# Optimization experiments

Measured on AMD Instinct MI355X. Metric: run time of the kernel, lower is better.

Reference implementation:

```python
import jax, jax.numpy as jnp
import numpy as np

B, S = 64, 256           # batch, seq_len
V, E = 50000, 256        # vocab, embedding dim
H, L = 256, 9            # lstm hidden, num labels


def setup_inputs() -> dict:
    key = jax.random.key(0)
    ks = jax.random.split(key, 12)
    inputs = jax.random.randint(ks[0], (B, S), 0, V, dtype=jnp.int32)
    attention_mask = jnp.ones((B, S), dtype=jnp.int32)
    label = jax.random.randint(ks[1], (B, S), 0, L, dtype=jnp.int32)
    emb = jax.random.normal(ks[2], (V, E), jnp.float32) * 0.02
    # LSTM weights, keras gate order: i, f, g(cell), o stacked along last axis
    W_fwd = jax.random.normal(ks[3], (E, 4 * H), jnp.float32) * 0.05
    U_fwd = jax.random.normal(ks[4], (H, 4 * H), jnp.float32) * 0.05
    b_fwd = jnp.zeros((4 * H,), jnp.float32)
    W_bwd = jax.random.normal(ks[5], (E, 4 * H), jnp.float32) * 0.05
    U_bwd = jax.random.normal(ks[6], (H, 4 * H), jnp.float32) * 0.05
    b_bwd = jnp.zeros((4 * H,), jnp.float32)
    W_dense = jax.random.normal(ks[7], (2 * H, L), jnp.float32) * 0.05
    b_dense = jnp.zeros((L,), jnp.float32)
    trans = jax.random.uniform(ks[8], (L, L), jnp.float32)  # tf.random.uniform init
    return dict(inputs=inputs, attention_mask=attention_mask, label=label,
                emb=emb, W_fwd=W_fwd, U_fwd=U_fwd, b_fwd=b_fwd,
                W_bwd=W_bwd, U_bwd=U_bwd, b_bwd=b_bwd,
                W_dense=W_dense, b_dense=b_dense, trans=trans)


def _lstm(x, W, U, b):
    # x: [B,S,E] -> h sequence [B,S,H]; keras default activations (sigmoid/tanh)
    Bx = x.shape[0]
    Hd = U.shape[0]
    xz = jnp.einsum('bse,ef->bsf', x, W) + b  # precompute input projection

    def step(carry, zt):
        h, c = carry
        z = zt + h @ U
        i, f, g, o = jnp.split(z, 4, axis=-1)
        c = jax.nn.sigmoid(f) * c + jax.nn.sigmoid(i) * jnp.tanh(g)
        h = jax.nn.sigmoid(o) * jnp.tanh(c)
        return (h, c), h

    init = (jnp.zeros((Bx, Hd), x.dtype), jnp.zeros((Bx, Hd), x.dtype))
    _, hs = jax.lax.scan(step, init, jnp.swapaxes(xz, 0, 1))
    return jnp.swapaxes(hs, 0, 1)


def _crf_log_likelihood(logits, tags, lengths, trans):
    # logits [B,S,L], tags [B,S] int, lengths [B] int, trans [L,L]
    Bx, Sx, Lx = logits.shape
    t_idx = jnp.arange(Sx)
    valid = (t_idx[None, :] < lengths[:, None]).astype(logits.dtype)  # [B,S]
    unary = jnp.take_along_axis(logits, tags[..., None], axis=-1)[..., 0]
    unary_score = jnp.sum(unary * valid, axis=1)
    pair_valid = (t_idx[None, :Sx - 1] < (lengths[:, None] - 1)).astype(logits.dtype)
    binary = trans[tags[:, :-1], tags[:, 1:]]
    binary_score = jnp.sum(binary * pair_valid, axis=1)

    # forward algorithm (log-space), masked so alpha is carried through padding
    alpha0 = logits[:, 0]  # [B,L]

    def step(alpha, inp):
        emit, m = inp  # emit [B,L], m [B] bool
        new = jax.nn.logsumexp(alpha[:, :, None] + trans[None], axis=1) + emit
        alpha = jnp.where(m[:, None], new, alpha)
        return alpha, None

    emits = jnp.swapaxes(logits[:, 1:], 0, 1)               # [S-1,B,L]
    masks = jnp.swapaxes(t_idx[None, 1:] < lengths[:, None], 0, 1)
    alpha, _ = jax.lax.scan(step, alpha0, (emits, masks))
    log_norm = jax.nn.logsumexp(alpha, axis=-1)
    return unary_score + binary_score - log_norm


def reference(inputs, attention_mask, label, emb, W_fwd, U_fwd, b_fwd,
              W_bwd, U_bwd, b_bwd, W_dense, b_dense, trans):
    x = emb[inputs]  # [B,S,E]; dropout is identity at inference (training=None)
    h_f = _lstm(x, W_fwd, U_fwd, b_fwd)
    h_b = _lstm(x[:, ::-1], W_bwd, U_bwd, b_bwd)[:, ::-1]
    h = jnp.concatenate([h_f, h_b], axis=-1)  # [B,S,2H]
    logits = h @ W_dense + b_dense            # [B,S,L]
    lengths = jnp.sum((attention_mask != 0).astype(jnp.int32), axis=1)
    log_likelihood = _crf_log_likelihood(logits, label, lengths, trans)
    return logits, log_likelihood, trans
```

## Files before the change

kernel.cpp:

```cpp
#include <hip/hip_runtime.h>
#include <hip/hip_fp16.h>

typedef _Float16 half2_t __attribute__((ext_vector_type(2)));
typedef unsigned int u32;

constexpr int Bn = 64, Sn = 256, Ln = 9;
constexpr int G4H = 1024;

constexpr size_t XZ_OFF   = 0;
constexpr size_t XZ_BYTES = (size_t)2 * Bn * Sn * G4H * 4;
constexpr size_t H_OFF    = XZ_OFF + XZ_BYTES;
constexpr size_t H_BYTES  = (size_t)Bn * Sn * 512 * 4;
constexpr size_t UPK_OFF  = H_OFF + H_BYTES;
constexpr size_t UPK_BYTES= (size_t)2 * 128 * G4H * 4;

constexpr int PV = 96;
constexpr int PL = 32;

__device__ __forceinline__ float sigf(float x) {
  return __fdividef(1.0f, 1.0f + __expf(-x));
}
__device__ __forceinline__ float tanhf_fast(float x) {
  x = fminf(fmaxf(x, -15.0f), 15.0f);
  float e = __expf(-2.0f * x);
  return __fdividef(1.0f - e, 1.0f + e);
}

#if __has_builtin(__builtin_amdgcn_fdot2)
__device__ __forceinline__ float FDOT2(half2_t a, half2_t b, float c) {
  return __builtin_amdgcn_fdot2(a, b, c, false);
}
#else
__device__ __forceinline__ float FDOT2(half2_t a, half2_t b, float c) {
  return c + (float)a.x * (float)b.x + (float)a.y * (float)b.y;
}
#endif

__device__ __forceinline__ half2_t H2(u32 w) { return __builtin_bit_cast(half2_t, w); }

__global__ void pack_u(const float* __restrict__ Uf, const float* __restrict__ Ub,
                       u32* __restrict__ upk) {
  int idx = blockIdx.x * 256 + threadIdx.x;
  if (idx >= 2 * 128 * 1024) return;
  int d  = idx >> 17;
  int kp = (idx >> 10) & 127;
  int j  = idx & 1023;
  const float* U = d ? Ub : Uf;
  _Float16 a = (_Float16)U[(size_t)(2 * kp) * 1024 + j];
  _Float16 b = (_Float16)U[(size_t)(2 * kp + 1) * 1024 + j];
  u32 pa = (u32)__builtin_bit_cast(unsigned short, a);
  u32 pb = (u32)__builtin_bit_cast(unsigned short, b);
  upk[idx] = pa | (pb << 16);
}

__global__ __launch_bounds__(256, 4)
void xz_gemm(const int* __restrict__ tok, const float* __restrict__ emb,
             const float* __restrict__ Wf, const float* __restrict__ biasf,
             const float* __restrict__ Wb, const float* __restrict__ biasb,
             float* __restrict__ xz) {
  __shared__ float As[32][64];
  __shared__ float Bs[32][128];
  __shared__ int toks[64];
  const int tid = threadIdx.x;
  const int mt = blockIdx.x, nt = blockIdx.y;
  const int d = nt >> 3;
  const float* W    = d ? Wb : Wf;
  const float* bias = d ? biasb : biasf;
  const int n0 = (nt & 7) * 128;
  const int r0 = mt * 64;
  if (tid < 64) toks[tid] = tok[r0 + tid];
  __syncthreads();
  const int tr = tid >> 4, tc = tid & 15;
  float acc[4][8];
#pragma unroll
  for (int j = 0; j < 8; ++j) {
    float bv = bias[n0 + tc * 8 + j];
#pragma unroll
    for (int i = 0; i < 4; ++i) acc[i][j] = bv;
  }
  const int ai = tid >> 2, kq = tid & 3;
  const int kb = tid >> 3, fb = tid & 7;
  for (int k0 = 0; k0 < 256; k0 += 32) {
    const float* ar = emb + (size_t)toks[ai] * 256 + k0 + kq * 8;
    float4 a0 = *(const float4*)ar;
    float4 a1 = *(const float4*)(ar + 4);
    As[kq * 8 + 0][ai] = a0.x; As[kq * 8 + 1][ai] = a0.y;
    As[kq * 8 + 2][ai] = a0.z; As[kq * 8 + 3][ai] = a0.w;
    As[kq * 8 + 4][ai] = a1.x; As[kq * 8 + 5][ai] = a1.y;
    As[kq * 8 + 6][ai] = a1.z; As[kq * 8 + 7][ai] = a1.w;
    const float* wr = W + (size_t)(k0 + kb) * 1024 + n0;
#pragma unroll
    for (int q = 0; q < 4; ++q)
      *(float4*)&Bs[kb][(fb + 8 * q) * 4] = *(const float4*)(wr + (fb + 8 * q) * 4);
    __syncthreads();
#pragma unroll
    for (int kk = 0; kk < 32; ++kk) {
      float4 a4 = *(const float4*)&As[kk][tr * 4];
      float4 b0 = *(const float4*)&Bs[kk][tc * 8];
      float4 b1 = *(const float4*)&Bs[kk][tc * 8 + 4];
      float av[4] = {a4.x, a4.y, a4.z, a4.w};
      float bv[8] = {b0.x, b0.y, b0.z, b0.w, b1.x, b1.y, b1.z, b1.w};
#pragma unroll
      for (int i = 0; i < 4; ++i)
#pragma unroll
        for (int j = 0; j < 8; ++j) acc[i][j] += av[i] * bv[j];
    }
    __syncthreads();
  }
#pragma unroll
  for (int i = 0; i < 4; ++i) {
    int r = r0 + tr * 4 + i;
    int bb_ = r >> 8, s = r & 255;
    float* dst = xz + ((size_t)(d * 64 + bb_) * 256 + s) * 1024 + n0 + tc * 8;
    float4 o0 = {acc[i][0], acc[i][1], acc[i][2], acc[i][3]};
    float4 o1 = {acc[i][4], acc[i][5], acc[i][6], acc[i][7]};
    *(float4*)dst = o0;
    *(float4*)(dst + 4) = o1;
  }
}

__global__ __launch_bounds__(512)
void lstm_seq(const float* __restrict__ xz, const u32* __restrict__ upk,
              float* __restrict__ h_out) {
  const int seq = blockIdx.x;
  const int dir = seq >> 6;
  const int tid = threadIdx.x;
  const int colA = tid;
  const int colB = tid + 512;

  __shared__ uint4 ul[2 * (PL / 4) * 512];
  __shared__ float zbuf[1024];
  __shared__ __align__(16) u32 h2[128];

  const u32* ubase = upk + (size_t)dir * 131072;

  half2_t uA[PV], uB[PV];
#pragma unroll
  for (int kp = 0; kp < PV; ++kp) {
    uA[kp] = H2(ubase[(size_t)kp * 1024 + colA]);
    uB[kp] = H2(ubase[(size_t)kp * 1024 + colB]);
  }
#pragma unroll
  for (int q = 0; q < PL / 4; ++q) {
    uint4 va, vb;
    va.x = ubase[(size_t)(PV + 4 * q + 0) * 1024 + colA];
    va.y = ubase[(size_t)(PV + 4 * q + 1) * 1024 + colA];
    va.z = ubase[(size_t)(PV + 4 * q + 2) * 1024 + colA];
    va.w = ubase[(size_t)(PV + 4 * q + 3) * 1024 + colA];
    vb.x = ubase[(size_t)(PV + 4 * q + 0) * 1024 + colB];
    vb.y = ubase[(size_t)(PV + 4 * q + 1) * 1024 + colB];
    vb.z = ubase[(size_t)(PV + 4 * q + 2) * 1024 + colB];
    vb.w = ubase[(size_t)(PV + 4 * q + 3) * 1024 + colB];
    ul[q * 512 + tid] = va;
    ul[(PL / 4 + q) * 512 + tid] = vb;
  }
  if (tid < 128) h2[tid] = 0u;
  float c = 0.0f;

  const float* xzp = xz + (size_t)seq * 256 * 1024;
  float* hop = h_out + (size_t)(seq & 63) * 256 * 512 + dir * 256 + tid;
  __syncthreads();

  float xA = xzp[(size_t)(dir ? 255 : 0) * 1024 + colA];
  float xB = xzp[(size_t)(dir ? 255 : 0) * 1024 + colB];

  for (int t = 0; t < 256; ++t) {
    const int snext = (t < 255) ? (dir ? (254 - t) : (t + 1)) : (dir ? 255 : 0);
    float nA = xzp[(size_t)snext * 1024 + colA];
    float nB = xzp[(size_t)snext * 1024 + colB];

    float accA = xA, accB = xB;
#pragma unroll
    for (int q = 0; q < PV / 4; ++q) {
      uint4 hh = *(const uint4*)&h2[4 * q];
      accA = FDOT2(H2(hh.x), uA[4 * q + 0], accA);
      accA = FDOT2(H2(hh.y), uA[4 * q + 1], accA);
      accA = FDOT2(H2(hh.z), uA[4 * q + 2], accA);
      accA = FDOT2(H2(hh.w), uA[4 * q + 3], accA);
      accB = FDOT2(H2(hh.x), uB[4 * q + 0], accB);
      accB = FDOT2(H2(hh.y), uB[4 * q + 1], accB);
      accB = FDOT2(H2(hh.z), uB[4 * q + 2], accB);
      accB = FDOT2(H2(hh.w), uB[4 * q + 3], accB);
    }
#pragma unroll
    for (int q = 0; q < PL / 4; ++q) {
      uint4 hh = *(const uint4*)&h2[PV + 4 * q];
      uint4 va = ul[q * 512 + tid];
      uint4 vb = ul[(PL / 4 + q) * 512 + tid];
      accA = FDOT2(H2(hh.x), H2(va.x), accA);
      accA = FDOT2(H2(hh.y), H2(va.y), accA);
      accA = FDOT2(H2(hh.z), H2(va.z), accA);
      accA = FDOT2(H2(hh.w), H2(va.w), accA);
      accB = FDOT2(H2(hh.x), H2(vb.x), accB);
      accB = FDOT2(H2(hh.y), H2(vb.y), accB);
      accB = FDOT2(H2(hh.z), H2(vb.z), accB);
      accB = FDOT2(H2(hh.w), H2(vb.w), accB);
    }
    zbuf[colA] = accA;
    zbuf[colB] = accB;
    __syncthreads();

    const int s = dir ? (255 - t) : t;
    if (tid < 256) {
      float zi = zbuf[tid], zf = zbuf[tid + 256], zg = zbuf[tid + 512], zo = zbuf[tid + 768];
      c = sigf(zf) * c + sigf(zi) * tanhf_fast(zg);
      float h = sigf(zo) * tanhf_fast(c);
      hop[(size_t)s * 512] = h;
      ((_Float16*)h2)[tid] = (_Float16)h;
    }
    __syncthreads();
    xA = nA; xB = nB;
  }
}

__global__ __launch_bounds__(256, 4)
void logits_k(const float* __restrict__ h_out, const float* __restrict__ Wd,
              const float* __restrict__ bd, float* __restrict__ out) {
  __shared__ float Ws[512 * 9];
  __shared__ float bs[16];
  const int tid = threadIdx.x;
  for (int i = tid; i < 4608; i += 256) Ws[i] = Wd[i];
  if (tid < 9) bs[tid] = bd[tid];
  __syncthreads();
  const int w = tid >> 6, lane = tid & 63;
  const int r0 = blockIdx.x * 16 + w * 4;
  for (int rr = 0; rr < 4; ++rr) {
    const int r = r0 + rr;
    const float* hp = h_out + (size_t)r * 512 + lane * 8;
    float4 h0 = *(const float4*)hp;
    float4 h1 = *(const float4*)(hp + 4);
    float hv[8] = {h0.x, h0.y, h0.z, h0.w, h1.x, h1.y, h1.z, h1.w};
    float outv = 0.0f;
#pragma unroll
    for (int l = 0; l < 9; ++l) {
      float p = 0.0f;
#pragma unroll
      for (int uu = 0; uu < 8; ++uu) p += hv[uu] * Ws[(lane * 8 + uu) * 9 + l];
      for (int off = 32; off; off >>= 1) p += __shfl_xor(p, off, 64);
      if (lane == l) outv = p;
    }
    if (lane < 9) out[(size_t)r * 9 + lane] = outv + bs[lane];
  }
}

__global__ void crf_k(const float* __restrict__ logits, const int* __restrict__ label,
                      const int* __restrict__ mask, const float* __restrict__ trans,
                      float* __restrict__ out_ll, float* __restrict__ out_trans) {
  const int b = blockIdx.x;
  const int lane = threadIdx.x;
  int cnt = 0;
#pragma unroll
  for (int q = 0; q < 4; ++q) cnt += (mask[b * 256 + lane + q * 64] != 0) ? 1 : 0;
  for (int off = 32; off; off >>= 1) cnt += __shfl_xor(cnt, off, 64);
  const int len = cnt;
  float un = 0.0f;
#pragma unroll
  for (int q = 0; q < 4; ++q) {
    int s = lane + q * 64;
    if (s < len) un += logits[((size_t)b * 256 + s) * 9 + label[b * 256 + s]];
  }
  for (int off = 32; off; off >>= 1) un += __shfl_xor(un, off, 64);
  float bin = 0.0f;
#pragma unroll
  for (int q = 0; q < 4; ++q) {
    int s = lane + q * 64;
    if (s < 255 && s < len - 1)
      bin += trans[label[b * 256 + s] * 9 + label[b * 256 + s + 1]];
  }
  for (int off = 32; off; off >>= 1) bin += __shfl_xor(bin, off, 64);
  float alpha = (lane < 9) ? logits[((size_t)b * 256) * 9 + lane] : -INFINITY;
  float tcol[9];
  if (lane < 9) {
#pragma unroll
    for (int i = 0; i < 9; ++i) tcol[i] = trans[i * 9 + lane];
  }
  for (int t = 1; t < 256; ++t) {
    float a[9];
#pragma unroll
    for (int i = 0; i < 9; ++i) a[i] = __shfl(alpha, i, 64);
    if (lane < 9) {
      float mx = a[0] + tcol[0];
#pragma unroll
      for (int i = 1; i < 9; ++i) mx = fmaxf(mx, a[i] + tcol[i]);
      float ssum = 0.0f;
#pragma unroll
      for (int i = 0; i < 9; ++i) ssum += __expf(a[i] + tcol[i] - mx);
      float nw = mx + __logf(ssum) + logits[((size_t)b * 256 + t) * 9 + lane];
      if (t < len) alpha = nw;
    }
  }
  float mx = alpha;
  for (int off = 32; off; off >>= 1) mx = fmaxf(mx, __shfl_xor(mx, off, 64));
  float e = __expf(alpha - mx);
  for (int off = 32; off; off >>= 1) e += __shfl_xor(e, off, 64);
  if (lane == 0) out_ll[b] = un + bin - (mx + __logf(e));
  if (b == 0) {
    for (int i = lane; i < 81; i += 64) out_trans[i] = trans[i];
  }
}

extern "C" void kernel_launch(void* const* d_in, const int* in_sizes, int n_in,
                              void* d_out, int out_size, void* d_ws, size_t ws_size,
                              hipStream_t stream) {
  (void)in_sizes; (void)n_in; (void)out_size; (void)ws_size;
  const int*   inputs = (const int*)d_in[0];
  const int*   amask  = (const int*)d_in[1];
  const int*   label  = (const int*)d_in[2];
  const float* emb    = (const float*)d_in[3];
  const float* Wf     = (const float*)d_in[4];
  const float* Uf     = (const float*)d_in[5];
  const float* bf     = (const float*)d_in[6];
  const float* Wb     = (const float*)d_in[7];
  const float* Ub     = (const float*)d_in[8];
  const float* bb     = (const float*)d_in[9];
  const float* Wd     = (const float*)d_in[10];
  const float* bd     = (const float*)d_in[11];
  const float* trans  = (const float*)d_in[12];

  char* ws = (char*)d_ws;
  float* xz    = (float*)(ws + XZ_OFF);
  float* h_out = (float*)(ws + H_OFF);
  u32*   upk   = (u32*)(ws + UPK_OFF);

  float* out      = (float*)d_out;
  float* out_ll   = out + (size_t)Bn * Sn * Ln;
  float* out_tr   = out_ll + Bn;

  pack_u<<<1024, 256, 0, stream>>>(Uf, Ub, upk);
  xz_gemm<<<dim3(256, 16), 256, 0, stream>>>(inputs, emb, Wf, bf, Wb, bb, xz);
  lstm_seq<<<128, 512, 0, stream>>>(xz, upk, h_out);
  logits_k<<<1024, 256, 0, stream>>>(h_out, Wd, bd, out);
  crf_k<<<64, 64, 0, stream>>>(out, label, amask, trans, out_ll, out_tr);
}
```

Baseline: 783.1 us.

## Split LSTM recurrent matvec across 4-lane K groups with swizzled h buffer

Each thread now owns 8 gate columns over a quarter of the hidden dimension instead of 2 full columns. Six of those columns' weights stay in registers and two sit in LDS, and the partial sums are combined with cross-lane shuffles. The fp16 hidden-state buffer is stored in a swizzled layout so each lane group reads distinct 16-byte chunks, avoiding LDS bank conflicts on the broadcast reads. The xz input is loaded as float4 vectors. The aim is more register reuse of each loaded h chunk and fewer LDS reads per step, at the cost of shuffle-reduction overhead and a fixed waves-per-EU hint.

```diff
diff --git a/kernel.cpp b/kernel.cpp
--- a/kernel.cpp
+++ b/kernel.cpp
@@ -14,9 +14,6 @@
 constexpr size_t UPK_OFF  = H_OFF + H_BYTES;
 constexpr size_t UPK_BYTES= (size_t)2 * 128 * G4H * 4;
 
-constexpr int PV = 96;
-constexpr int PL = 32;
-
 __device__ __forceinline__ float sigf(float x) {
   return __fdividef(1.0f, 1.0f + __expf(-x));
 }
@@ -37,6 +34,10 @@
 #endif
 
 __device__ __forceinline__ half2_t H2(u32 w) { return __builtin_bit_cast(half2_t, w); }
+
+__device__ __forceinline__ int swz_g(int g) {
+  return (g & 24) | ((g + 2 * (g >> 3)) & 7);
+}
 
 __global__ void pack_u(const float* __restrict__ Uf, const float* __restrict__ Ub,
                        u32* __restrict__ upk) {
@@ -120,96 +121,115 @@
 }
 
 __global__ __launch_bounds__(512)
+__attribute__((amdgpu_waves_per_eu(2, 2)))
 void lstm_seq(const float* __restrict__ xz, const u32* __restrict__ upk,
               float* __restrict__ h_out) {
   const int seq = blockIdx.x;
   const int dir = seq >> 6;
   const int tid = threadIdx.x;
-  const int colA = tid;
-  const int colB = tid + 512;
-
-  __shared__ uint4 ul[2 * (PL / 4) * 512];
+  const int w    = tid >> 6;
+  const int lane = tid & 63;
+  const int kb   = lane & 3;
+  const int cb   = lane >> 2;
+  const int c0   = w * 128 + cb * 8;
+
+  __shared__ uint4 ul[16][512];
   __shared__ float zbuf[1024];
   __shared__ __align__(16) u32 h2[128];
 
-  const u32* ubase = upk + (size_t)dir * 131072;
-
-  half2_t uA[PV], uB[PV];
-#pragma unroll
-  for (int kp = 0; kp < PV; ++kp) {
-    uA[kp] = H2(ubase[(size_t)kp * 1024 + colA]);
-    uB[kp] = H2(ubase[(size_t)kp * 1024 + colB]);
-  }
-#pragma unroll
-  for (int q = 0; q < PL / 4; ++q) {
-    uint4 va, vb;
-    va.x = ubase[(size_t)(PV + 4 * q + 0) * 1024 + colA];
-    va.y = ubase[(size_t)(PV + 4 * q + 1) * 1024 + colA];
-    va.z = ubase[(size_t)(PV + 4 * q + 2) * 1024 + colA];
-    va.w = ubase[(size_t)(PV + 4 * q + 3) * 1024 + colA];
-    vb.x = ubase[(size_t)(PV + 4 * q + 0) * 1024 + colB];
-    vb.y = ubase[(size_t)(PV + 4 * q + 1) * 1024 + colB];
-    vb.z = ubase[(size_t)(PV + 4 * q + 2) * 1024 + colB];
-    vb.w = ubase[(size_t)(PV + 4 * q + 3) * 1024 + colB];
-    ul[q * 512 + tid] = va;
-    ul[(PL / 4 + q) * 512 + tid] = vb;
-  }
+  const u32* ub = upk + (size_t)dir * 131072;
+
+  half2_t uu[6][32];
+#pragma unroll
+  for (int j = 0; j < 6; ++j)
+#pragma unroll
+    for (int q = 0; q < 32; ++q)
+      uu[j][q] = H2(ub[(size_t)(32 * kb + q) * 1024 + (c0 + j)]);
+#pragma unroll
+  for (int j = 0; j < 6; ++j)
+#pragma unroll
+    for (int q = 0; q < 32; ++q)
+      asm volatile("" : "+v"(uu[j][q]));
+
+#pragma unroll
+  for (int cl = 0; cl < 2; ++cl)
+#pragma unroll
+    for (int s = 0; s < 8; ++s) {
+      uint4 v;
+      v.x = ub[(size_t)(32 * kb + 4 * s + 0) * 1024 + (c0 + 6 + cl)];
+      v.y = ub[(size_t)(32 * kb + 4 * s + 1) * 1024 + (c0 + 6 + cl)];
+      v.z = ub[(size_t)(32 * kb + 4 * s + 2) * 1024 + (c0 + 6 + cl)];
+      v.w = ub[(size_t)(32 * kb + 4 * s + 3) * 1024 + (c0 + 6 + cl)];
+      ul[cl * 8 + s][tid] = v;
+    }
   if (tid < 128) h2[tid] = 0u;
+
+  const char* h2b = (const char*)h2;
+  int hhoff[8];
+#pragma unroll
+  for (int s = 0; s < 8; ++s)
+    hhoff[s] = 16 * ((kb << 3) | ((s + 2 * kb) & 7));
+
   float c = 0.0f;
-
-  const float* xzp = xz + (size_t)seq * 256 * 1024;
+  char* hwp = (char*)h2 + (swz_g(tid >> 3) * 16 + (tid & 7) * 2);
   float* hop = h_out + (size_t)(seq & 63) * 256 * 512 + dir * 256 + tid;
+
+  const float* xzp = xz + (size_t)seq * 256 * 1024 + c0;
   __syncthreads();
 
-  float xA = xzp[(size_t)(dir ? 255 : 0) * 1024 + colA];
-  float xB = xzp[(size_t)(dir ? 255 : 0) * 1024 + colB];
+  float4 xc0 = *(const float4*)(xzp + (size_t)(dir ? 255 : 0) * 1024);
+  float4 xc1 = *(const float4*)(xzp + (size_t)(dir ? 255 : 0) * 1024 + 4);
 
   for (int t = 0; t < 256; ++t) {
+    const int scur = dir ? (255 - t) : t;
     const int snext = (t < 255) ? (dir ? (254 - t) : (t + 1)) : (dir ? 255 : 0);
-    float nA = xzp[(size_t)snext * 1024 + colA];
-    float nB = xzp[(size_t)snext * 1024 + colB];
-
-    float accA = xA, accB = xB;
-#pragma unroll
-    for (int q = 0; q < PV / 4; ++q) {
-      uint4 hh = *(const uint4*)&h2[4 * q];
-      accA = FDOT2(H2(hh.x), uA[4 * q + 0], accA);
-      accA = FDOT2(H2(hh.y), uA[4 * q + 1], accA);
-      accA = FDOT2(H2(hh.z), uA[4 * q + 2], accA);
-      accA = FDOT2(H2(hh.w), uA[4 * q + 3], accA);
-      accB = FDOT2(H2(hh.x), uB[4 * q + 0], accB);
-      accB = FDOT2(H2(hh.y), uB[4 * q + 1], accB);
-      accB = FDOT2(H2(hh.z), uB[4 * q + 2], accB);
-      accB = FDOT2(H2(hh.w), uB[4 * q + 3], accB);
-    }
-#pragma unroll
-    for (int q = 0; q < PL / 4; ++q) {
-      uint4 hh = *(const uint4*)&h2[PV + 4 * q];
-      uint4 va = ul[q * 512 + tid];
-      uint4 vb = ul[(PL / 4 + q) * 512 + tid];
-      accA = FDOT2(H2(hh.x), H2(va.x), accA);
-      accA = FDOT2(H2(hh.y), H2(va.y), accA);
-      accA = FDOT2(H2(hh.z), H2(va.z), accA);
-      accA = FDOT2(H2(hh.w), H2(va.w), accA);
-      accB = FDOT2(H2(hh.x), H2(vb.x), accB);
-      accB = FDOT2(H2(hh.y), H2(vb.y), accB);
-      accB = FDOT2(H2(hh.z), H2(vb.z), accB);
-      accB = FDOT2(H2(hh.w), H2(vb.w), accB);
-    }
-    zbuf[colA] = accA;
-    zbuf[colB] = accB;
+    float4 nx0 = *(const float4*)(xzp + (size_t)snext * 1024);
+    float4 nx1 = *(const float4*)(xzp + (size_t)snext * 1024 + 4);
+
+    float acc[8] = {0.f, 0.f, 0.f, 0.f, 0.f, 0.f, 0.f, 0.f};
+#pragma unroll
+    for (int s = 0; s < 8; ++s) {
+      uint4 hh = *(const uint4*)(h2b + hhoff[s]);
+      uint4 va = ul[s][tid];
+      uint4 vb = ul[8 + s][tid];
+#pragma unroll
+      for (int j = 0; j < 6; ++j) {
+        acc[j] = FDOT2(H2(hh.x), uu[j][4 * s + 0], acc[j]);
+        acc[j] = FDOT2(H2(hh.y), uu[j][4 * s + 1], acc[j]);
+        acc[j] = FDOT2(H2(hh.z), uu[j][4 * s + 2], acc[j]);
+        acc[j] = FDOT2(H2(hh.w), uu[j][4 * s + 3], acc[j]);
+      }
+      acc[6] = FDOT2(H2(hh.x), H2(va.x), acc[6]);
+      acc[6] = FDOT2(H2(hh.y), H2(va.y), acc[6]);
+      acc[6] = FDOT2(H2(hh.z), H2(va.z), acc[6]);
+      acc[6] = FDOT2(H2(hh.w), H2(va.w), acc[6]);
+      acc[7] = FDOT2(H2(hh.x), H2(vb.x), acc[7]);
+      acc[7] = FDOT2(H2(hh.y), H2(vb.y), acc[7]);
+      acc[7] = FDOT2(H2(hh.z), H2(vb.z), acc[7]);
+      acc[7] = FDOT2(H2(hh.w), H2(vb.w), acc[7]);
+    }
+#pragma unroll
+    for (int j = 0; j < 8; ++j) {
+      acc[j] += __shfl_xor(acc[j], 1, 64);
+      acc[j] += __shfl_xor(acc[j], 2, 64);
+    }
+    if (kb == 0) {
+      float4 z0 = {acc[0] + xc0.x, acc[1] + xc0.y, acc[2] + xc0.z, acc[3] + xc0.w};
+      float4 z1 = {acc[4] + xc1.x, acc[5] + xc1.y, acc[6] + xc1.z, acc[7] + xc1.w};
+      *(float4*)&zbuf[c0] = z0;
+      *(float4*)&zbuf[c0 + 4] = z1;
+    }
     __syncthreads();
 
-    const int s = dir ? (255 - t) : t;
     if (tid < 256) {
       float zi = zbuf[tid], zf = zbuf[tid + 256], zg = zbuf[tid + 512], zo = zbuf[tid + 768];
       c = sigf(zf) * c + sigf(zi) * tanhf_fast(zg);
       float h = sigf(zo) * tanhf_fast(c);
-      hop[(size_t)s * 512] = h;
-      ((_Float16*)h2)[tid] = (_Float16)h;
+      hop[(size_t)scur * 512] = h;
+      *(_Float16*)hwp = (_Float16)h;
     }
     __syncthreads();
-    xA = nA; xB = nB;
+    xc0 = nx0; xc1 = nx1;
   }
 }
 
```

After: 762.1 us. 1.03x faster.

## Quantize LSTM recurrent weights to FP8 and use fp32 hidden state

Applied to the files above, without the earlier changes.

Packs the recurrent matrices U into FP8 (four values per 32-bit word) rather than fp16 pairs. That halves the register and LDS footprint for the weights: 40 words stay in registers and 24 in LDS per column. The inner loop unpacks the FP8 values to fp32 and runs packed fp32 multiply-adds against an fp32 hidden state, replacing the fdot2 instructions. The aim is to cut register pressure and weight load traffic in the sequential LSTM kernel, at the cost of extra conversion instructions and a large loss of weight precision that may break accuracy tolerances.

```diff
diff --git a/kernel.cpp b/kernel.cpp
--- a/kernel.cpp
+++ b/kernel.cpp
@@ -1,7 +1,7 @@
 #include <hip/hip_runtime.h>
 #include <hip/hip_fp16.h>
 
-typedef _Float16 half2_t __attribute__((ext_vector_type(2)));
+typedef float f32x2 __attribute__((ext_vector_type(2)));
 typedef unsigned int u32;
 
 constexpr int Bn = 64, Sn = 256, Ln = 9;
@@ -11,11 +11,11 @@
 constexpr size_t XZ_BYTES = (size_t)2 * Bn * Sn * G4H * 4;
 constexpr size_t H_OFF    = XZ_OFF + XZ_BYTES;
 constexpr size_t H_BYTES  = (size_t)Bn * Sn * 512 * 4;
-constexpr size_t UPK_OFF  = H_OFF + H_BYTES;
-constexpr size_t UPK_BYTES= (size_t)2 * 128 * G4H * 4;
-
-constexpr int PV = 96;
-constexpr int PL = 32;
+constexpr size_t U8_OFF   = H_OFF + H_BYTES;
+constexpr size_t U8_BYTES = (size_t)2 * 64 * G4H * 4;
+
+constexpr int RQ = 40;
+constexpr int LQ = 24;
 
 __device__ __forceinline__ float sigf(float x) {
   return __fdividef(1.0f, 1.0f + __expf(-x));
@@ -26,31 +26,61 @@
   return __fdividef(1.0f - e, 1.0f + e);
 }
 
-#if __has_builtin(__builtin_amdgcn_fdot2)
-__device__ __forceinline__ float FDOT2(half2_t a, half2_t b, float c) {
-  return __builtin_amdgcn_fdot2(a, b, c, false);
-}
+#if __has_builtin(__builtin_amdgcn_cvt_pk_f32_fp8)
+#define CVT2LO(w) ((f32x2)__builtin_amdgcn_cvt_pk_f32_fp8((w), false))
+#define CVT2HI(w) ((f32x2)__builtin_amdgcn_cvt_pk_f32_fp8((w), true))
 #else
-__device__ __forceinline__ float FDOT2(half2_t a, half2_t b, float c) {
-  return c + (float)a.x * (float)b.x + (float)a.y * (float)b.y;
+__device__ __forceinline__ float dec8(u32 x) {
+  u32 s = x >> 7, e = (x >> 3) & 15, m = x & 7;
+  float v = (e == 0) ? (float)m * 0.001953125f : ldexpf((float)(8 + m), (int)e - 10);
+  return s ? -v : v;
+}
+__device__ __forceinline__ f32x2 CVT2LO(u32 w) {
+  return (f32x2){dec8(w & 0xff), dec8((w >> 8) & 0xff)};
+}
+__device__ __forceinline__ f32x2 CVT2HI(u32 w) {
+  return (f32x2){dec8((w >> 16) & 0xff), dec8(w >> 24)};
 }
 #endif
 
-__device__ __forceinline__ half2_t H2(u32 w) { return __builtin_bit_cast(half2_t, w); }
-
-__global__ void pack_u(const float* __restrict__ Uf, const float* __restrict__ Ub,
-                       u32* __restrict__ upk) {
+__device__ __forceinline__ u32 enc8(float f) {
+  u32 s = signbit(f) ? 0x80u : 0u;
+  float a = fabsf(f);
+  if (!(a > 0.f)) return s;
+  if (a >= 448.f) return s | 0x7E;
+  if (a < 0.015625f) {
+    int m = (int)rintf(a * 512.f);
+    if (m > 7) return s | 0x08;
+    return s | (u32)m;
+  }
+  int e; float fr = frexpf(a, &e);
+  int m = (int)rintf((fr * 2.f - 1.f) * 8.f);
+  int E = e + 6;
+  if (m == 8) { m = 0; E += 1; }
+  if (E >= 16) return s | 0x7E;
+  return s | ((u32)E << 3) | (u32)m;
+}
+
+__global__ void pack_u8(const float* __restrict__ Uf, const float* __restrict__ Ub,
+                        u32* __restrict__ u8) {
   int idx = blockIdx.x * 256 + threadIdx.x;
-  if (idx >= 2 * 128 * 1024) return;
-  int d  = idx >> 17;
-  int kp = (idx >> 10) & 127;
-  int j  = idx & 1023;
+  if (idx >= 2 * 64 * 1024) return;
+  int d = idx >> 16;
+  int q = (idx >> 10) & 63;
+  int j = idx & 1023;
   const float* U = d ? Ub : Uf;
-  _Float16 a = (_Float16)U[(size_t)(2 * kp) * 1024 + j];
-  _Float16 b = (_Float16)U[(size_t)(2 * kp + 1) * 1024 + j];
-  u32 pa = (u32)__builtin_bit_cast(unsigned short, a);
-  u32 pb = (u32)__builtin_bit_cast(unsigned short, b);
-  upk[idx] = pa | (pb << 16);
+  float a = U[(size_t)(4 * q + 0) * 1024 + j];
+  float b = U[(size_t)(4 * q + 1) * 1024 + j];
+  float c = U[(size_t)(4 * q + 2) * 1024 + j];
+  float e = U[(size_t)(4 * q + 3) * 1024 + j];
+#if __has_builtin(__builtin_amdgcn_cvt_pk_fp8_f32)
+  int v = 0;
+  v = __builtin_amdgcn_cvt_pk_fp8_f32(a, b, v, false);
+  v = __builtin_amdgcn_cvt_pk_fp8_f32(c, e, v, true);
+  u8[idx] = (u32)v;
+#else
+  u8[idx] = enc8(a) | (enc8(b) << 8) | (enc8(c) << 16) | (enc8(e) << 24);
+#endif
 }
 
 __global__ __launch_bounds__(256, 4)
@@ -120,7 +150,7 @@
 }
 
 __global__ __launch_bounds__(512)
-void lstm_seq(const float* __restrict__ xz, const u32* __restrict__ upk,
+void lstm_seq(const float* __restrict__ xz, const u32* __restrict__ u8,
               float* __restrict__ h_out) {
   const int seq = blockIdx.x;
   const int dir = seq >> 6;
@@ -128,35 +158,36 @@
   const int colA = tid;
   const int colB = tid + 512;
 
-  __shared__ uint4 ul[2 * (PL / 4) * 512];
+  __shared__ uint4 ulA4[LQ / 4][512];
+  __shared__ uint4 ulB4[LQ / 4][512];
   __shared__ float zbuf[1024];
-  __shared__ __align__(16) u32 h2[128];
-
-  const u32* ubase = upk + (size_t)dir * 131072;
-
-  half2_t uA[PV], uB[PV];
-#pragma unroll
-  for (int kp = 0; kp < PV; ++kp) {
-    uA[kp] = H2(ubase[(size_t)kp * 1024 + colA]);
-    uB[kp] = H2(ubase[(size_t)kp * 1024 + colB]);
-  }
-#pragma unroll
-  for (int q = 0; q < PL / 4; ++q) {
+  __shared__ __align__(16) float h32[256];
+
+  const u32* ub = u8 + (size_t)dir * 65536;
+
+  u32 uqA[RQ], uqB[RQ];
+#pragma unroll
+  for (int q = 0; q < RQ; ++q) {
+    uqA[q] = ub[(size_t)q * 1024 + colA];
+    uqB[q] = ub[(size_t)q * 1024 + colB];
+  }
+#pragma unroll
+  for (int r = 0; r < LQ / 4; ++r) {
     uint4 va, vb;
-    va.x = ubase[(size_t)(PV + 4 * q + 0) * 1024 + colA];
-    va.y = ubase[(size_t)(PV + 4 * q + 1) * 1024 + colA];
-    va.z = ubase[(size_t)(PV + 4 * q + 2) * 1024 + colA];
-    va.w = ubase[(size_t)(PV + 4 * q + 3) * 1024 + colA];
-    vb.x = ubase[(size_t)(PV + 4 * q + 0) * 1024 + colB];
-    vb.y = ubase[(size_t)(PV + 4 * q + 1) * 1024 + colB];
-    vb.z = ubase[(size_t)(PV + 4 * q + 2) * 1024 + colB];
-    vb.w = ubase[(size_t)(PV + 4 * q + 3) * 1024 + colB];
-    ul[q * 512 + tid] = va;
-    ul[(PL / 4 + q) * 512 + tid] = vb;
-  }
-  if (tid < 128) h2[tid] = 0u;
+    va.x = ub[(size_t)(RQ + 4 * r + 0) * 1024 + colA];
+    va.y = ub[(size_t)(RQ + 4 * r + 1) * 1024 + colA];
+    va.z = ub[(size_t)(RQ + 4 * r + 2) * 1024 + colA];
+    va.w = ub[(size_t)(RQ + 4 * r + 3) * 1024 + colA];
+    vb.x = ub[(size_t)(RQ + 4 * r + 0) * 1024 + colB];
+    vb.y = ub[(size_t)(RQ + 4 * r + 1) * 1024 + colB];
+    vb.z = ub[(size_t)(RQ + 4 * r + 2) * 1024 + colB];
+    vb.w = ub[(size_t)(RQ + 4 * r + 3) * 1024 + colB];
+    ulA4[r][tid] = va;
+    ulB4[r][tid] = vb;
+  }
+  if (tid < 256) h32[tid] = 0.0f;
+
   float c = 0.0f;
-
   const float* xzp = xz + (size_t)seq * 256 * 1024;
   float* hop = h_out + (size_t)(seq & 63) * 256 * 512 + dir * 256 + tid;
   __syncthreads();
@@ -165,48 +196,63 @@
   float xB = xzp[(size_t)(dir ? 255 : 0) * 1024 + colB];
 
   for (int t = 0; t < 256; ++t) {
+    const int scur = dir ? (255 - t) : t;
     const int snext = (t < 255) ? (dir ? (254 - t) : (t + 1)) : (dir ? 255 : 0);
     float nA = xzp[(size_t)snext * 1024 + colA];
     float nB = xzp[(size_t)snext * 1024 + colB];
 
-    float accA = xA, accB = xB;
-#pragma unroll
-    for (int q = 0; q < PV / 4; ++q) {
-      uint4 hh = *(const uint4*)&h2[4 * q];
-      accA = FDOT2(H2(hh.x), uA[4 * q + 0], accA);
-      accA = FDOT2(H2(hh.y), uA[4 * q + 1], accA);
-      accA = FDOT2(H2(hh.z), uA[4 * q + 2], accA);
-      accA = FDOT2(H2(hh.w), uA[4 * q + 3], accA);
-      accB = FDOT2(H2(hh.x), uB[4 * q + 0], accB);
-      accB = FDOT2(H2(hh.y), uB[4 * q + 1], accB);
-      accB = FDOT2(H2(hh.z), uB[4 * q + 2], accB);
-      accB = FDOT2(H2(hh.w), uB[4 * q + 3], accB);
-    }
-#pragma unroll
-    for (int q = 0; q < PL / 4; ++q) {
-      uint4 hh = *(const uint4*)&h2[PV + 4 * q];
-      uint4 va = ul[q * 512 + tid];
-      uint4 vb = ul[(PL / 4 + q) * 512 + tid];
-      accA = FDOT2(H2(hh.x), H2(va.x), accA);
-      accA = FDOT2(H2(hh.y), H2(va.y), accA);
-      accA = FDOT2(H2(hh.z), H2(va.z), accA);
-      accA = FDOT2(H2(hh.w), H2(va.w), accA);
-      accB = FDOT2(H2(hh.x), H2(vb.x), accB);
-      accB = FDOT2(H2(hh.y), H2(vb.y), accB);
-      accB = FDOT2(H2(hh.z), H2(vb.z), accB);
-      accB = FDOT2(H2(hh.w), H2(vb.w), accB);
-    }
-    zbuf[colA] = accA;
-    zbuf[colB] = accB;
+    f32x2 aA = {xA, 0.0f};
+    f32x2 aB = {xB, 0.0f};
+#pragma unroll
+    for (int q = 0; q < RQ; ++q) {
+      float4 hq = *(const float4*)&h32[4 * q];
+      f32x2 h01 = {hq.x, hq.y};
+      f32x2 h23 = {hq.z, hq.w};
+      aA += CVT2LO(uqA[q]) * h01;
+      aA += CVT2HI(uqA[q]) * h23;
+      aB += CVT2LO(uqB[q]) * h01;
+      aB += CVT2HI(uqB[q]) * h23;
+    }
+#pragma unroll
+    for (int r = 0; r < LQ / 4; ++r) {
+      uint4 va = ulA4[r][tid];
+      uint4 vb = ulB4[r][tid];
+      const int qb = RQ + 4 * r;
+      {
+        float4 hq = *(const float4*)&h32[4 * (qb + 0)];
+        f32x2 h01 = {hq.x, hq.y}, h23 = {hq.z, hq.w};
+        aA += CVT2LO(va.x) * h01; aA += CVT2HI(va.x) * h23;
+        aB += CVT2LO(vb.x) * h01; aB += CVT2HI(vb.x) * h23;
+      }
+      {
+        float4 hq = *(const float4*)&h32[4 * (qb + 1)];
+        f32x2 h01 = {hq.x, hq.y}, h23 = {hq.z, hq.w};
+        aA += CVT2LO(va.y) * h01; aA += CVT2HI(va.y) * h23;
+        aB += CVT2LO(vb.y) * h01; aB += CVT2HI(vb.y) * h23;
+      }
+      {
+        float4 hq = *(const float4*)&h32[4 * (qb + 2)];
+        f32x2 h01 = {hq.x, hq.y}, h23 = {hq.z, hq.w};
+        aA += CVT2LO(va.z) * h01; aA += CVT2HI(va.z) * h23;
+        aB += CVT2LO(vb.z) * h01; aB += CVT2HI(vb.z) * h23;
+      }
+      {
+        float4 hq = *(const float4*)&h32[4 * (qb + 3)];
+        f32x2 h01 = {hq.x, hq.y}, h23 = {hq.z, hq.w};
+        aA += CVT2LO(va.w) * h01; aA += CVT2HI(va.w) * h23;
+        aB += CVT2LO(vb.w) * h01; aB += CVT2HI(vb.w) * h23;
+      }
+    }
+    zbuf[colA] = aA.x + aA.y;
+    zbuf[colB] = aB.x + aB.y;
     __syncthreads();
 
-    const int s = dir ? (255 - t) : t;
     if (tid < 256) {
       float zi = zbuf[tid], zf = zbuf[tid + 256], zg = zbuf[tid + 512], zo = zbuf[tid + 768];
       c = sigf(zf) * c + sigf(zi) * tanhf_fast(zg);
       float h = sigf(zo) * tanhf_fast(c);
-      hop[(size_t)s * 512] = h;
-      ((_Float16*)h2)[tid] = (_Float16)h;
+      hop[(size_t)scur * 512] = h;
+      h32[tid] = h;
     }
     __syncthreads();
     xA = nA; xB = nB;
@@ -320,15 +366,15 @@
   char* ws = (char*)d_ws;
   float* xz    = (float*)(ws + XZ_OFF);
   float* h_out = (float*)(ws + H_OFF);
-  u32*   upk   = (u32*)(ws + UPK_OFF);
+  u32*   u8    = (u32*)(ws + U8_OFF);
 
   float* out      = (float*)d_out;
   float* out_ll   = out + (size_t)Bn * Sn * Ln;
   float* out_tr   = out_ll + Bn;
 
-  pack_u<<<1024, 256, 0, stream>>>(Uf, Ub, upk);
+  pack_u8<<<512, 256, 0, stream>>>(Uf, Ub, u8);
   xz_gemm<<<dim3(256, 16), 256, 0, stream>>>(inputs, emb, Wf, bf, Wb, bb, xz);
-  lstm_seq<<<128, 512, 0, stream>>>(xz, upk, h_out);
+  lstm_seq<<<128, 512, 0, stream>>>(xz, u8, h_out);
   logits_k<<<1024, 256, 0, stream>>>(h_out, Wd, bd, out);
   crf_k<<<64, 64, 0, stream>>>(out, label, amask, trans, out_ll, out_tr);
 }
```

New measurement: 2.295 ms. +193.0%, slower.
